# Kernel optimization log

Measured on AMD Instinct MI355X. Metric: run time of the kernel, lower is better.

## Reference

```python
import jax, jax.numpy as jnp
import numpy as np

H = 512      # config.hidden_dim
N = 64       # batch
W = 512      # sentence length
K = 8        # decode steps = pointer_answers.size(1)
NEG_BIG = 1e10


def setup_inputs() -> dict:
    key = jax.random.key(0)
    ks = jax.random.split(key, 10)
    stdv = 1.0 / np.sqrt(H)
    u = lambda k_, shape, s: jax.random.uniform(k_, shape, jnp.float32, -s, s)
    return {
        "context": jax.random.normal(ks[0], (N, W, 2 * H), jnp.float32),
        "sentence_lens": jax.random.randint(ks[1], (N,), 1, W + 1),
        "pointer_answers": jax.random.randint(ks[2], (N, K), 0, W + 1),
        "V_w": u(ks[3], (H, 2 * H), 1.0 / np.sqrt(2 * H)),
        "W_w": u(ks[4], (H, H), stdv),
        "v": u(ks[5], (H,), stdv),
        "w_ih": u(ks[6], (3 * H, 2 * H), stdv),
        "w_hh": u(ks[7], (3 * H, H), stdv),
        "b_ih": u(ks[8], (3 * H,), stdv),
        "b_hh": u(ks[9], (3 * H,), stdv),
    }


def reference(context, sentence_lens, pointer_answers, V_w, W_w, v, w_ih, w_hh, b_ih, b_hh):
    n, w_len, two_h = context.shape
    h_dim = two_h // 2
    k = pointer_answers.shape[1]

    # encoder output permuted to (W, N, 2H)
    ctx = jnp.swapaxes(context, 0, 1)
    # faithful reproduction of: context_new[i] = (1 - (i >= lens+1)*1e10) * context[i]
    pos = jnp.arange(w_len)[:, None]                                  # (W, 1)
    factor = 1.0 - (pos >= sentence_lens[None, :] + 1).astype(context.dtype) * NEG_BIG  # (W, N)
    ctx_masked = ctx * factor[:, :, None]                             # (W, N, 2H)
    # appended zeros row -> (W+1, N, 2H)
    context_new = jnp.concatenate([ctx_masked, jnp.zeros((1, n, two_h), context.dtype)], axis=0)

    ctx_t = jnp.einsum('snd,hd->snh', context_new, V_w)               # (W+1, N, H) = V(context_new)

    h0 = jnp.zeros((n, h_dim), context.dtype)

    def step(h, _):
        f = jnp.tanh(ctx_t + (h @ W_w.T)[None])                       # (W+1, N, H)
        scores = jnp.einsum('snh,h->sn', f, v)                        # (W+1, N)
        beta = jax.nn.softmax(scores, axis=0)                         # softmax over positions
        aligned = jnp.einsum('sn,snd->nd', beta, context_new)         # (N, 2H)
        # torch GRUCell math
        gi = aligned @ w_ih.T + b_ih                                  # (N, 3H)
        gh = h @ w_hh.T + b_hh                                        # (N, 3H)
        ir, iz, inew = jnp.split(gi, 3, axis=1)
        hr, hz, hnew = jnp.split(gh, 3, axis=1)
        r = jax.nn.sigmoid(ir + hr)
        z = jax.nn.sigmoid(iz + hz)
        ncand = jnp.tanh(inew + r * hnew)
        h_new = (1.0 - z) * ncand + z * h
        return h_new, beta.T                                          # (N, W+1)

    _, betas = jax.lax.scan(step, h0, None, length=k)                 # (k, N, W+1)
    # torch: cat over steps then permute -> (N, k, W+1) -> (N*k, W+1)
    out = jnp.transpose(betas, (1, 0, 2)).reshape(n * k, w_len + 1)
    return out
```

## Files before the change

kernel.cpp:

```cpp
#include <hip/hip_runtime.h>

#define N_    64
#define W_    512
#define H_    512
#define S_    513
#define TWOH_ 1024
#define KS_   8
#define FIXCAP_ 131072

typedef short s16x8 __attribute__((ext_vector_type(8)));
typedef float f32x4 __attribute__((ext_vector_type(4)));
typedef _Float16 h16x8 __attribute__((ext_vector_type(8)));

__device__ __forceinline__ float tanh_fast(float x) {
  float xc = fminf(fmaxf(x, -15.0f), 15.0f);
  float e = __expf(2.0f * xc);
  return (e - 1.0f) / (e + 1.0f);
}
__device__ __forceinline__ float sigmoid_f(float x) {
  return 1.0f / (1.0f + __expf(-x));
}
__device__ __forceinline__ float wred_sum(float v) {
#pragma unroll
  for (int m = 32; m > 0; m >>= 1) v += __shfl_xor(v, m, 64);
  return v;
}
__device__ __forceinline__ float bf2f(unsigned short u) {
  return __uint_as_float(((unsigned)u) << 16);
}

__device__ __forceinline__ void gld_lds16(const void* g, void* s) {
  __builtin_amdgcn_global_load_lds((__attribute__((address_space(1))) void*)g,
                                   (__attribute__((address_space(3))) void*)s,
                                   16, 0, 0);
}

__global__ __launch_bounds__(256) void k_cvt(const float4* __restrict__ x,
                                             unsigned short* __restrict__ hi,
                                             unsigned short* __restrict__ lo,
                                             int n4) {
  for (int i = blockIdx.x * 256 + threadIdx.x; i < n4; i += gridDim.x * 256) {
    float4 v = x[i];
    float vs[4] = {v.x, v.y, v.z, v.w};
    unsigned short hb[4], lb[4];
#pragma unroll
    for (int j = 0; j < 4; ++j) {
      unsigned u = __float_as_uint(vs[j]);
      unsigned short h = (unsigned short)((u + 0x7FFFu + ((u >> 16) & 1u)) >> 16);
      float hf = __uint_as_float((unsigned)h << 16);
      float lf = vs[j] - hf;
      unsigned u2 = __float_as_uint(lf);
      unsigned short l = (unsigned short)((u2 + 0x7FFFu + ((u2 >> 16) & 1u)) >> 16);
      hb[j] = h; lb[j] = l;
    }
    ushort4 h4; h4.x = hb[0]; h4.y = hb[1]; h4.z = hb[2]; h4.w = hb[3];
    ushort4 l4; l4.x = lb[0]; l4.y = lb[1]; l4.z = lb[2]; l4.w = lb[3];
    ((ushort4*)hi)[i] = h4;
    ((ushort4*)lo)[i] = l4;
  }
}

__global__ __launch_bounds__(256, 2) void mfma_gemm(
    const unsigned short* __restrict__ Ahi, const unsigned short* __restrict__ Alo,
    const unsigned short* __restrict__ Bhi, const unsigned short* __restrict__ Blo,
    _Float16* __restrict__ C) {
  __shared__ unsigned short sAh[4096], sAl[4096], sBh[4096], sBl[4096];
  int bid = blockIdx.x;
  int swz = (bid & 7) * 128 + (bid >> 3);
  int mt = swz >> 2, nt = swz & 3;
  int m0 = mt * 128, n0 = nt * 128;
  int tid = threadIdx.x;
  int wave = tid >> 6, lane = tid & 63;
  int wr = wave >> 1, wc = wave & 1;
  int fr = lane & 15, fq = lane >> 4;
  int rA = tid >> 2;
  int cA = (tid & 3) * 8;

  f32x4 acc[4][4] = {};

  const size_t a_row0 = (size_t)(m0 + rA) << 10;
  const size_t a_row1 = (size_t)(m0 + rA + 64) << 10;
  const size_t b_row0 = (size_t)(n0 + rA) << 10;
  const size_t b_row1 = (size_t)(n0 + rA + 64) << 10;
  const int wofs = wave << 9;

  for (int k0 = 0; k0 < 1024; k0 += 32) {
    int off = k0 + cA;
    gld_lds16(Ahi + a_row0 + off, sAh + wofs);
    gld_lds16(Ahi + a_row1 + off, sAh + 2048 + wofs);
    gld_lds16(Alo + a_row0 + off, sAl + wofs);
    gld_lds16(Alo + a_row1 + off, sAl + 2048 + wofs);
    gld_lds16(Bhi + b_row0 + off, sBh + wofs);
    gld_lds16(Bhi + b_row1 + off, sBh + 2048 + wofs);
    gld_lds16(Blo + b_row0 + off, sBl + wofs);
    gld_lds16(Blo + b_row1 + off, sBl + 2048 + wofs);
    __syncthreads();
    s16x8 ah[4], av[4], bh[4], bv[4];
#pragma unroll
    for (int m = 0; m < 4; ++m) {
      int ar = (wr * 64 + m * 16 + fr) * 32 + fq * 8;
      ah[m] = *(const s16x8*)(sAh + ar);
      av[m] = *(const s16x8*)(sAl + ar);
    }
#pragma unroll
    for (int n = 0; n < 4; ++n) {
      int br = (wc * 64 + n * 16 + fr) * 32 + fq * 8;
      bh[n] = *(const s16x8*)(sBh + br);
      bv[n] = *(const s16x8*)(sBl + br);
    }
#pragma unroll
    for (int m = 0; m < 4; ++m)
#pragma unroll
      for (int n = 0; n < 4; ++n) {
        acc[m][n] = __builtin_amdgcn_mfma_f32_16x16x32_bf16(ah[m], bh[n], acc[m][n], 0, 0, 0);
        acc[m][n] = __builtin_amdgcn_mfma_f32_16x16x32_bf16(ah[m], bv[n], acc[m][n], 0, 0, 0);
        acc[m][n] = __builtin_amdgcn_mfma_f32_16x16x32_bf16(av[m], bh[n], acc[m][n], 0, 0, 0);
      }
    __syncthreads();
  }
#pragma unroll
  for (int m = 0; m < 4; ++m) {
    int gr0 = m0 + wr * 64 + m * 16 + fq * 4;
#pragma unroll
    for (int n = 0; n < 4; ++n) {
      int gc = n0 + wc * 64 + n * 16 + fr;
      _Float16* cp = C + (size_t)gr0 * 512 + gc;
#pragma unroll
      for (int r = 0; r < 4; ++r) cp[(size_t)r * 512] = (_Float16)acc[m][n][r];
    }
  }
}

__global__ __launch_bounds__(1024) void k_mscore(
    const int* __restrict__ slens, const float* __restrict__ vvec,
    const _Float16* __restrict__ Vc16, float* __restrict__ scores,
    int* __restrict__ fixcnt, int* __restrict__ fixlist) {
  int nb = blockIdx.x & 63, cb = blockIdx.x >> 6;
  int t = threadIdx.x;
  int len = slens[nb];
  int w = t >> 6, lane = t & 63;
  int hb = lane << 3;
  float4 v0 = *(const float4*)(vvec + hb);
  float4 v1 = *(const float4*)(vvec + hb + 4);
  float vv[8] = {v0.x, v0.y, v0.z, v0.w, v1.x, v1.y, v1.z, v1.w};
  int s0 = max(cb * 128, len + 1);
  int s_end = min((cb + 1) * 128, W_);
  for (int s = s0 + w; s < s_end; s += 16) {
    h16x8 x8 = *(const h16x8*)(Vc16 + ((size_t)nb * W_ + s) * H_ + hb);
    float acc = 0.0f;
#pragma unroll
    for (int i = 0; i < 8; ++i) {
      float vcv = (float)x8[i];
      if (fabsf(vcv) < 6e-5f) {
        int idx = atomicAdd(fixcnt, 1);
        if (idx < FIXCAP_) fixlist[idx] = (nb << 20) | (s << 10) | (hb + i);
      } else {
        acc += (vcv > 0.0f) ? -vv[i] : vv[i];
      }
    }
    acc = wred_sum(acc);
    if (lane == 0) scores[nb * S_ + s] = acc;
  }
}

__global__ __launch_bounds__(256) void k_fix(
    const float* __restrict__ ctx, const float* __restrict__ Vw,
    const float* __restrict__ vvec, const int* __restrict__ fixcnt,
    const int* __restrict__ fixlist, float* __restrict__ scores) {
  int wid = (blockIdx.x * 256 + threadIdx.x) >> 6;
  int lane = threadIdx.x & 63;
  int cnt = min(*fixcnt, FIXCAP_);
  for (int e = wid; e < cnt; e += 1024) {
    int pk = fixlist[e];
    int n = pk >> 20, s = (pk >> 10) & 1023, h = pk & 1023;
    const float* cr = ctx + ((size_t)n * W_ + s) * TWOH_ + lane * 16;
    const float* wr = Vw + (size_t)h * TWOH_ + lane * 16;
    double acc = 0.0;
#pragma unroll
    for (int i = 0; i < 16; ++i) acc += (double)cr[i] * (double)wr[i];
#pragma unroll
    for (int m = 32; m > 0; m >>= 1) acc += __shfl_xor(acc, m, 64);
    if (lane == 0) {
      float vh = vvec[h];
      float contrib = (acc > 0.0) ? -vh : ((acc < 0.0) ? vh : 0.0f);
      if (contrib != 0.0f) atomicAdd(&scores[n * S_ + s], contrib);
    }
  }
}

__global__ __launch_bounds__(1024) void k_prep2(
    const float* __restrict__ ctx, const int* __restrict__ slens,
    const float* __restrict__ scores, float* __restrict__ Cmask) {
  __shared__ float4 red4[16 * 64];
  int nb = blockIdx.x & 63, cb = blockIdx.x >> 6;
  int t = threadIdx.x;
  int len = slens[nb];
  int dl = t & 63, sl = t >> 6;
  int d4 = cb * 256 + dl * 4;
  const float4* cp = (const float4*)(ctx + (size_t)nb * W_ * TWOH_) + (d4 >> 2);
  float4 acc = make_float4(0.f, 0.f, 0.f, 0.f);
#pragma unroll 4
  for (int s = len + 1 + sl; s < W_; s += 16) {
    float ew = __expf(scores[nb * S_ + s]);
    float4 c4 = cp[(size_t)s * (TWOH_ / 4)];
    acc.x += ew * c4.x; acc.y += ew * c4.y;
    acc.z += ew * c4.z; acc.w += ew * c4.w;
  }
  red4[sl * 64 + dl] = acc;
  __syncthreads();
  if (sl == 0) {
    float4 s4 = red4[dl];
#pragma unroll
    for (int i = 1; i < 16; ++i) {
      float4 o = red4[i * 64 + dl];
      s4.x += o.x; s4.y += o.y; s4.z += o.z; s4.w += o.w;
    }
    s4.x *= -1.0e10f; s4.y *= -1.0e10f; s4.z *= -1.0e10f; s4.w *= -1.0e10f;
    *(float4*)(Cmask + nb * TWOH_ + d4) = s4;
  }
}

__global__ __launch_bounds__(1024) void k_hw(const float* __restrict__ hc,
                                             const float* __restrict__ Ww,
                                             float* __restrict__ hWb) {
  __shared__ float ww[8][512];
  int b = blockIdx.x;
  int t = threadIdx.x;
  int h0 = b * 8;
  for (int i = t; i < 8 * 512; i += 1024)
    ww[i >> 9][i & 511] = Ww[(size_t)(h0 + (i >> 9)) * H_ + (i & 511)];
  __syncthreads();
  int lane = t & 63;
  int hl = (t >> 6) & 7;
  int nh = t >> 9;
  const float* wr = &ww[hl][lane << 3];
  float4 w0 = *(const float4*)wr;
  float4 w1 = *(const float4*)(wr + 4);
  for (int n = nh * 32; n < nh * 32 + 32; n += 2) {
    const float* hr0 = hc + (size_t)n * H_ + (lane << 3);
    const float* hr1 = hr0 + H_;
    float4 a0 = *(const float4*)hr0;
    float4 a1 = *(const float4*)(hr0 + 4);
    float4 b0 = *(const float4*)hr1;
    float4 b1 = *(const float4*)(hr1 + 4);
    float acc0 = a0.x * w0.x + a0.y * w0.y + a0.z * w0.z + a0.w * w0.w +
                 a1.x * w1.x + a1.y * w1.y + a1.z * w1.z + a1.w * w1.w;
    float acc1 = b0.x * w0.x + b0.y * w0.y + b0.z * w0.z + b0.w * w0.w +
                 b1.x * w1.x + b1.y * w1.y + b1.z * w1.z + b1.w * w1.w;
    acc0 = wred_sum(acc0);
    acc1 = wred_sum(acc1);
    if (lane == 0) {
      hWb[(size_t)n * H_ + h0 + hl] = acc0;
      hWb[(size_t)(n + 1) * H_ + h0 + hl] = acc1;
    }
  }
}

__global__ __launch_bounds__(1024) void k_scores(
    const int* __restrict__ slens, const float* __restrict__ hWb,
    const _Float16* __restrict__ Vc16, const float* __restrict__ vvec,
    float* __restrict__ scores) {
  int nb = blockIdx.x & 63, cb = blockIdx.x >> 6;
  int t = threadIdx.x;
  int len = slens[nb];
  int smax = min(len, W_ - 1);
  int w = t >> 6, lane = t & 63;
  int hb = lane << 3;
  float4 h0 = *(const float4*)(hWb + nb * H_ + hb);
  float4 h1 = *(const float4*)(hWb + nb * H_ + hb + 4);
  float4 v0 = *(const float4*)(vvec + hb);
  float4 v1 = *(const float4*)(vvec + hb + 4);
  float hw[8] = {h0.x, h0.y, h0.z, h0.w, h1.x, h1.y, h1.z, h1.w};
  float vv[8] = {v0.x, v0.y, v0.z, v0.w, v1.x, v1.y, v1.z, v1.w};
  int s_end = min((cb + 1) * 128 - 1, smax);
  const _Float16* vcb = Vc16 + (size_t)nb * W_ * H_ + hb;
  int s = cb * 128 + w;
  for (; s + 48 <= s_end; s += 64) {
    h16x8 x0 = *(const h16x8*)(vcb + (size_t)s * H_);
    h16x8 x1 = *(const h16x8*)(vcb + (size_t)(s + 16) * H_);
    h16x8 x2 = *(const h16x8*)(vcb + (size_t)(s + 32) * H_);
    h16x8 x3 = *(const h16x8*)(vcb + (size_t)(s + 48) * H_);
    float a0 = 0.f, a1 = 0.f, a2 = 0.f, a3 = 0.f;
#pragma unroll
    for (int i = 0; i < 8; ++i) {
      a0 += tanh_fast((float)x0[i] + hw[i]) * vv[i];
      a1 += tanh_fast((float)x1[i] + hw[i]) * vv[i];
      a2 += tanh_fast((float)x2[i] + hw[i]) * vv[i];
      a3 += tanh_fast((float)x3[i] + hw[i]) * vv[i];
    }
    a0 = wred_sum(a0); a1 = wred_sum(a1);
    a2 = wred_sum(a2); a3 = wred_sum(a3);
    if (lane == 0) {
      scores[nb * S_ + s] = a0;
      scores[nb * S_ + s + 16] = a1;
      scores[nb * S_ + s + 32] = a2;
      scores[nb * S_ + s + 48] = a3;
    }
  }
  for (; s <= s_end; s += 16) {
    h16x8 x8 = *(const h16x8*)(vcb + (size_t)s * H_);
    float acc = 0.0f;
#pragma unroll
    for (int i = 0; i < 8; ++i) acc += tanh_fast((float)x8[i] + hw[i]) * vv[i];
    acc = wred_sum(acc);
    if (lane == 0) scores[nb * S_ + s] = acc;
  }
  if (cb == 3 && w == 15) {
    float acc = 0.0f;
#pragma unroll
    for (int i = 0; i < 8; ++i) acc += tanh_fast(hw[i]) * vv[i];
    acc = wred_sum(acc);
    if (lane == 0) scores[nb * S_ + W_] = acc;
  }
}

__global__ __launch_bounds__(1024) void k_soft_aligned(
    const unsigned short* __restrict__ ctxb, const int* __restrict__ slens,
    const float* __restrict__ scores, const float* __restrict__ Cmask,
    float* __restrict__ alignedb, float* __restrict__ out, int k) {
  __shared__ float beta[520];
  __shared__ float wsum[16];
  __shared__ float redl[32 * 32 * 8];
  int nb = blockIdx.x & 63, cb = blockIdx.x >> 6;
  int t = threadIdx.x;
  int len = slens[nb];
  int smax = min(len, W_ - 1);

  float e = (t < S_) ? __expf(scores[nb * S_ + t]) : 0.0f;
  float ws_ = wred_sum(e);
  if ((t & 63) == 0) wsum[t >> 6] = ws_;
  __syncthreads();
  float D = 0.0f;
#pragma unroll
  for (int i = 0; i < 16; ++i) D += wsum[i];
  if (t < S_) {
    float bt = e / D;
    beta[t] = bt;
    if (cb == 0) out[(size_t)(nb * KS_ + k) * S_ + t] = bt;
  }
  __syncthreads();

  int dl = t & 31, sl = t >> 5;
  int d8 = cb * 256 + dl * 8;
  const unsigned short* cp = ctxb + (size_t)nb * W_ * TWOH_ + d8;
  float a[8] = {};
  int s = sl;
  for (; s + 96 <= smax; s += 128) {
    float b0 = beta[s], b1 = beta[s + 32], b2 = beta[s + 64], b3 = beta[s + 96];
    s16x8 c0 = *(const s16x8*)(cp + (size_t)s * TWOH_);
    s16x8 c1 = *(const s16x8*)(cp + (size_t)(s + 32) * TWOH_);
    s16x8 c2 = *(const s16x8*)(cp + (size_t)(s + 64) * TWOH_);
    s16x8 c3 = *(const s16x8*)(cp + (size_t)(s + 96) * TWOH_);
#pragma unroll
    for (int i = 0; i < 8; ++i)
      a[i] += b0 * bf2f((unsigned short)c0[i]) + b1 * bf2f((unsigned short)c1[i]) +
              b2 * bf2f((unsigned short)c2[i]) + b3 * bf2f((unsigned short)c3[i]);
  }
  for (; s <= smax; s += 32) {
    float bt = beta[s];
    s16x8 c = *(const s16x8*)(cp + (size_t)s * TWOH_);
#pragma unroll
    for (int i = 0; i < 8; ++i) a[i] += bt * bf2f((unsigned short)c[i]);
  }
  float4* rp = (float4*)(redl + (sl * 32 + dl) * 8);
  rp[0] = make_float4(a[0], a[1], a[2], a[3]);
  rp[1] = make_float4(a[4], a[5], a[6], a[7]);
  __syncthreads();
  if (t < 32) {
    float s8[8] = {};
#pragma unroll 8
    for (int q = 0; q < 32; ++q) {
      const float* p = redl + (q * 32 + t) * 8;
#pragma unroll
      for (int i = 0; i < 8; ++i) s8[i] += p[i];
    }
    float coef = 1.0f / D;
    int d8o = cb * 256 + t * 8;
    const float* cmp = Cmask + nb * TWOH_ + d8o;
    float* ap = alignedb + nb * TWOH_ + d8o;
#pragma unroll
    for (int i = 0; i < 8; ++i) ap[i] = s8[i] + coef * cmp[i];
  }
}

__global__ __launch_bounds__(1024) void k_gru(
    const float* __restrict__ alignedb, const float* __restrict__ hc,
    const float* __restrict__ wih, const float* __restrict__ whh,
    const float* __restrict__ bih, const float* __restrict__ bhh,
    float* __restrict__ hnx) {
  __shared__ float ls_wih[6 * TWOH_];
  __shared__ float ls_whh[6 * H_];
  __shared__ float part[8 * 128 * 6];
  int b = blockIdx.x;
  int t = threadIdx.x;
  const int j0 = 2 * b;
  for (int i = t; i < 6 * TWOH_; i += 1024) {
    int row = i >> 10, d = i & 1023;
    int jl = row / 3, g = row - jl * 3;
    ls_wih[i] = wih[(size_t)(g * H_ + j0 + jl) * TWOH_ + d];
  }
  for (int i = t; i < 6 * H_; i += 1024) {
    int row = i >> 9, d = i & 511;
    int jl = row / 3, g = row - jl * 3;
    ls_whh[i] = whh[(size_t)(g * H_ + j0 + jl) * H_ + d];
  }
  __syncthreads();
  int nj = t & 127, sl = t >> 7;
  int n = nj & 63, jl = nj >> 6;
  const float* ar = alignedb + n * TWOH_ + sl * 128;
  const float* hr = hc + n * H_ + sl * 64;
  const float* w0 = ls_wih + (jl * 3 + 0) * TWOH_ + sl * 128;
  const float* w1 = ls_wih + (jl * 3 + 1) * TWOH_ + sl * 128;
  const float* w2 = ls_wih + (jl * 3 + 2) * TWOH_ + sl * 128;
  const float* u0 = ls_whh + (jl * 3 + 0) * H_ + sl * 64;
  const float* u1 = ls_whh + (jl * 3 + 1) * H_ + sl * 64;
  const float* u2 = ls_whh + (jl * 3 + 2) * H_ + sl * 64;
  float g0 = 0.f, g1 = 0.f, g2 = 0.f;
#pragma unroll 8
  for (int i = 0; i < 128; i += 4) {
    float4 a4 = *(const float4*)(ar + i);
    g0 += a4.x * w0[i] + a4.y * w0[i + 1] + a4.z * w0[i + 2] + a4.w * w0[i + 3];
    g1 += a4.x * w1[i] + a4.y * w1[i + 1] + a4.z * w1[i + 2] + a4.w * w1[i + 3];
    g2 += a4.x * w2[i] + a4.y * w2[i + 1] + a4.z * w2[i + 2] + a4.w * w2[i + 3];
  }
  float q0 = 0.f, q1 = 0.f, q2 = 0.f;
#pragma unroll 8
  for (int i = 0; i < 64; i += 4) {
    float4 h4 = *(const float4*)(hr + i);
    q0 += h4.x * u0[i] + h4.y * u0[i + 1] + h4.z * u0[i + 2] + h4.w * u0[i + 3];
    q1 += h4.x * u1[i] + h4.y * u1[i + 1] + h4.z * u1[i + 2] + h4.w * u1[i + 3];
    q2 += h4.x * u2[i] + h4.y * u2[i + 1] + h4.z * u2[i + 2] + h4.w * u2[i + 3];
  }
  float* pp = part + (sl * 128 + nj) * 6;
  pp[0] = g0; pp[1] = g1; pp[2] = g2; pp[3] = q0; pp[4] = q1; pp[5] = q2;
  __syncthreads();
  if (t < 128) {
    int n2 = t & 63, jl2 = t >> 6;
    int j = j0 + jl2;
    float G0 = 0.f, G1 = 0.f, G2 = 0.f, Q0 = 0.f, Q1 = 0.f, Q2 = 0.f;
#pragma unroll
    for (int s = 0; s < 8; ++s) {
      float* p = part + (s * 128 + t) * 6;
      G0 += p[0]; G1 += p[1]; G2 += p[2];
      Q0 += p[3]; Q1 += p[4]; Q2 += p[5];
    }
    float r = sigmoid_f(G0 + bih[j] + Q0 + bhh[j]);
    float z = sigmoid_f(G1 + bih[H_ + j] + Q1 + bhh[H_ + j]);
    float nc = tanh_fast(G2 + bih[2 * H_ + j] + r * (Q2 + bhh[2 * H_ + j]));
    hnx[n2 * H_ + j] = (1.0f - z) * nc + z * hc[n2 * H_ + j];
  }
}

extern "C" void kernel_launch(void* const* d_in, const int* in_sizes, int n_in,
                              void* d_out, int out_size, void* d_ws, size_t ws_size,
                              hipStream_t stream) {
  const float* ctx = (const float*)d_in[0];
  const int* slens = (const int*)d_in[1];
  const float* Vw = (const float*)d_in[3];
  const float* Ww = (const float*)d_in[4];
  const float* vvec = (const float*)d_in[5];
  const float* wih = (const float*)d_in[6];
  const float* whh = (const float*)d_in[7];
  const float* bih = (const float*)d_in[8];
  const float* bhh = (const float*)d_in[9];
  float* out = (float*)d_out;

  char* p = (char*)d_ws;
  _Float16* Vc16 = (_Float16*)p;      p += (size_t)N_ * W_ * H_ * 2;
  float* scores = (float*)p;          p += (size_t)N_ * S_ * 4;
  int* fixcnt = (int*)p;              p += 256;
  int* fixlist = (int*)p;             p += (size_t)FIXCAP_ * 4;
  float* Cm = (float*)p;              p += (size_t)N_ * TWOH_ * 4;
  float* hb = (float*)p;              p += (size_t)2 * N_ * H_ * 4;
  float* hWb = (float*)p;             p += (size_t)N_ * H_ * 4;
  float* al = (float*)p;              p += (size_t)N_ * TWOH_ * 4;
  unsigned short* Ahi = (unsigned short*)p;  p += (size_t)32768 * 1024 * 2;
  unsigned short* Alo = (unsigned short*)p;  p += (size_t)32768 * 1024 * 2;
  unsigned short* Bhi = (unsigned short*)p;  p += (size_t)512 * 1024 * 2;
  unsigned short* Blo = (unsigned short*)p;  p += (size_t)512 * 1024 * 2;
  size_t need = (size_t)(p - (char*)d_ws);
  if (ws_size < need) return;

  hipMemsetAsync(hb, 0, (size_t)N_ * H_ * sizeof(float), stream);
  hipMemsetAsync(fixcnt, 0, sizeof(int), stream);
  k_cvt<<<2048, 256, 0, stream>>>((const float4*)ctx, Ahi, Alo, 8388608);
  k_cvt<<<512, 256, 0, stream>>>((const float4*)Vw, Bhi, Blo, 131072);
  mfma_gemm<<<1024, 256, 0, stream>>>(Ahi, Alo, Bhi, Blo, Vc16);
  k_mscore<<<256, 1024, 0, stream>>>(slens, vvec, Vc16, scores, fixcnt, fixlist);
  k_fix<<<256, 256, 0, stream>>>(ctx, Vw, vvec, fixcnt, fixlist, scores);
  k_prep2<<<256, 1024, 0, stream>>>(ctx, slens, scores, Cm);

  for (int k = 0; k < KS_; ++k) {
    const float* hc = hb + (k & 1) * (N_ * H_);
    float* hn = hb + ((k + 1) & 1) * (N_ * H_);
    k_hw<<<64, 1024, 0, stream>>>(hc, Ww, hWb);
    k_scores<<<256, 1024, 0, stream>>>(slens, hWb, Vc16, vvec, scores);
    k_soft_aligned<<<256, 1024, 0, stream>>>(Ahi, slens, scores, Cm, al, out, k);
    k_gru<<<256, 1024, 0, stream>>>(al, hc, wih, whh, bih, bhh, hn);
  }
}
```

Measured before the change: 692.7 us.

## Fuse masked-score pass into GEMM epilogue, merge conversions, double grid sizes

```diff
diff --git a/kernel.cpp b/kernel.cpp
--- a/kernel.cpp
+++ b/kernel.cpp
@@ -35,12 +35,15 @@
                                    16, 0, 0);
 }
 
-__global__ __launch_bounds__(256) void k_cvt(const float4* __restrict__ x,
-                                             unsigned short* __restrict__ hi,
-                                             unsigned short* __restrict__ lo,
-                                             int n4) {
-  for (int i = blockIdx.x * 256 + threadIdx.x; i < n4; i += gridDim.x * 256) {
-    float4 v = x[i];
+__global__ __launch_bounds__(256) void k_cvt2(
+    const float4* __restrict__ xa, unsigned short* __restrict__ Ahi,
+    unsigned short* __restrict__ Alo, const float4* __restrict__ xb,
+    unsigned short* __restrict__ Bhi, unsigned short* __restrict__ Blo) {
+  const int NA = 8388608;
+  const int NT = NA + 131072;
+  for (int i = blockIdx.x * 256 + threadIdx.x; i < NT; i += gridDim.x * 256) {
+    bool isA = (i < NA);
+    float4 v = isA ? xa[i] : xb[i - NA];
     float vs[4] = {v.x, v.y, v.z, v.w};
     unsigned short hb[4], lb[4];
 #pragma unroll
@@ -55,15 +58,22 @@
     }
     ushort4 h4; h4.x = hb[0]; h4.y = hb[1]; h4.z = hb[2]; h4.w = hb[3];
     ushort4 l4; l4.x = lb[0]; l4.y = lb[1]; l4.z = lb[2]; l4.w = lb[3];
-    ((ushort4*)hi)[i] = h4;
-    ((ushort4*)lo)[i] = l4;
+    if (isA) {
+      ((ushort4*)Ahi)[i] = h4;
+      ((ushort4*)Alo)[i] = l4;
+    } else {
+      ((ushort4*)Bhi)[i - NA] = h4;
+      ((ushort4*)Blo)[i - NA] = l4;
+    }
   }
 }
 
 __global__ __launch_bounds__(256, 2) void mfma_gemm(
     const unsigned short* __restrict__ Ahi, const unsigned short* __restrict__ Alo,
     const unsigned short* __restrict__ Bhi, const unsigned short* __restrict__ Blo,
-    _Float16* __restrict__ C) {
+    _Float16* __restrict__ C, const int* __restrict__ slens,
+    const float* __restrict__ vvec, float* __restrict__ scores,
+    int* __restrict__ fixcnt, int* __restrict__ fixlist) {
   __shared__ unsigned short sAh[4096], sAl[4096], sBh[4096], sBl[4096];
   int bid = blockIdx.x;
   int swz = (bid & 7) * 128 + (bid >> 3);
@@ -118,48 +128,50 @@
       }
     __syncthreads();
   }
+
+  const int n_batch = m0 >> 9;
+  const int len = slens[n_batch];
+  const int s_tile0 = m0 & 511;
+  const bool any_masked = (s_tile0 + 127 >= len + 1);
+  float vv4[4];
+#pragma unroll
+  for (int nf = 0; nf < 4; ++nf) vv4[nf] = vvec[n0 + wc * 64 + nf * 16 + fr];
+
 #pragma unroll
   for (int m = 0; m < 4; ++m) {
     int gr0 = m0 + wr * 64 + m * 16 + fq * 4;
 #pragma unroll
-    for (int n = 0; n < 4; ++n) {
-      int gc = n0 + wc * 64 + n * 16 + fr;
+    for (int nf = 0; nf < 4; ++nf) {
+      int gc = n0 + wc * 64 + nf * 16 + fr;
       _Float16* cp = C + (size_t)gr0 * 512 + gc;
 #pragma unroll
-      for (int r = 0; r < 4; ++r) cp[(size_t)r * 512] = (_Float16)acc[m][n][r];
-    }
-  }
-}
-
-__global__ __launch_bounds__(1024) void k_mscore(
-    const int* __restrict__ slens, const float* __restrict__ vvec,
-    const _Float16* __restrict__ Vc16, float* __restrict__ scores,
-    int* __restrict__ fixcnt, int* __restrict__ fixlist) {
-  int nb = blockIdx.x & 63, cb = blockIdx.x >> 6;
-  int t = threadIdx.x;
-  int len = slens[nb];
-  int w = t >> 6, lane = t & 63;
-  int hb = lane << 3;
-  float4 v0 = *(const float4*)(vvec + hb);
-  float4 v1 = *(const float4*)(vvec + hb + 4);
-  float vv[8] = {v0.x, v0.y, v0.z, v0.w, v1.x, v1.y, v1.z, v1.w};
-  int s0 = max(cb * 128, len + 1);
-  int s_end = min((cb + 1) * 128, W_);
-  for (int s = s0 + w; s < s_end; s += 16) {
-    h16x8 x8 = *(const h16x8*)(Vc16 + ((size_t)nb * W_ + s) * H_ + hb);
-    float acc = 0.0f;
-#pragma unroll
-    for (int i = 0; i < 8; ++i) {
-      float vcv = (float)x8[i];
-      if (fabsf(vcv) < 6e-5f) {
-        int idx = atomicAdd(fixcnt, 1);
-        if (idx < FIXCAP_) fixlist[idx] = (nb << 20) | (s << 10) | (hb + i);
-      } else {
-        acc += (vcv > 0.0f) ? -vv[i] : vv[i];
+      for (int r = 0; r < 4; ++r) cp[(size_t)r * 512] = (_Float16)acc[m][nf][r];
+    }
+    if (any_masked) {
+#pragma unroll
+      for (int r = 0; r < 4; ++r) {
+        int s_row = (gr0 + r) & 511;
+        if (s_row >= len + 1) {
+          float part = 0.0f;
+#pragma unroll
+          for (int nf = 0; nf < 4; ++nf) {
+            float a = acc[m][nf][r];
+            if (fabsf(a) <= 1e-5f) {
+              int gc = n0 + wc * 64 + nf * 16 + fr;
+              int idx = atomicAdd(fixcnt, 1);
+              if (idx < FIXCAP_) fixlist[idx] = (n_batch << 20) | (s_row << 10) | gc;
+            } else {
+              part += (a > 0.0f) ? -vv4[nf] : vv4[nf];
+            }
+          }
+          part += __shfl_xor(part, 1, 64);
+          part += __shfl_xor(part, 2, 64);
+          part += __shfl_xor(part, 4, 64);
+          part += __shfl_xor(part, 8, 64);
+          if (fr == 0) atomicAdd(&scores[n_batch * S_ + s_row], part);
+        }
       }
     }
-    acc = wred_sum(acc);
-    if (lane == 0) scores[nb * S_ + s] = acc;
   }
 }
 
@@ -223,20 +235,20 @@
 __global__ __launch_bounds__(1024) void k_hw(const float* __restrict__ hc,
                                              const float* __restrict__ Ww,
                                              float* __restrict__ hWb) {
-  __shared__ float ww[8][512];
+  __shared__ float ww[4][512];
   int b = blockIdx.x;
   int t = threadIdx.x;
-  int h0 = b * 8;
-  for (int i = t; i < 8 * 512; i += 1024)
+  int h0 = b * 4;
+  for (int i = t; i < 4 * 512; i += 1024)
     ww[i >> 9][i & 511] = Ww[(size_t)(h0 + (i >> 9)) * H_ + (i & 511)];
   __syncthreads();
   int lane = t & 63;
-  int hl = (t >> 6) & 7;
-  int nh = t >> 9;
+  int hl = (t >> 6) & 3;
+  int nh = t >> 8;
   const float* wr = &ww[hl][lane << 3];
   float4 w0 = *(const float4*)wr;
   float4 w1 = *(const float4*)(wr + 4);
-  for (int n = nh * 32; n < nh * 32 + 32; n += 2) {
+  for (int n = nh * 16; n < nh * 16 + 16; n += 2) {
     const float* hr0 = hc + (size_t)n * H_ + (lane << 3);
     const float* hr1 = hr0 + H_;
     float4 a0 = *(const float4*)hr0;
@@ -272,29 +284,22 @@
   float4 v1 = *(const float4*)(vvec + hb + 4);
   float hw[8] = {h0.x, h0.y, h0.z, h0.w, h1.x, h1.y, h1.z, h1.w};
   float vv[8] = {v0.x, v0.y, v0.z, v0.w, v1.x, v1.y, v1.z, v1.w};
-  int s_end = min((cb + 1) * 128 - 1, smax);
+  int s_end = min((cb + 1) * 64 - 1, smax);
   const _Float16* vcb = Vc16 + (size_t)nb * W_ * H_ + hb;
-  int s = cb * 128 + w;
-  for (; s + 48 <= s_end; s += 64) {
+  int s = cb * 64 + w;
+  for (; s + 16 <= s_end; s += 32) {
     h16x8 x0 = *(const h16x8*)(vcb + (size_t)s * H_);
     h16x8 x1 = *(const h16x8*)(vcb + (size_t)(s + 16) * H_);
-    h16x8 x2 = *(const h16x8*)(vcb + (size_t)(s + 32) * H_);
-    h16x8 x3 = *(const h16x8*)(vcb + (size_t)(s + 48) * H_);
-    float a0 = 0.f, a1 = 0.f, a2 = 0.f, a3 = 0.f;
+    float a0 = 0.f, a1 = 0.f;
 #pragma unroll
     for (int i = 0; i < 8; ++i) {
       a0 += tanh_fast((float)x0[i] + hw[i]) * vv[i];
       a1 += tanh_fast((float)x1[i] + hw[i]) * vv[i];
-      a2 += tanh_fast((float)x2[i] + hw[i]) * vv[i];
-      a3 += tanh_fast((float)x3[i] + hw[i]) * vv[i];
     }
     a0 = wred_sum(a0); a1 = wred_sum(a1);
-    a2 = wred_sum(a2); a3 = wred_sum(a3);
     if (lane == 0) {
       scores[nb * S_ + s] = a0;
       scores[nb * S_ + s + 16] = a1;
-      scores[nb * S_ + s + 32] = a2;
-      scores[nb * S_ + s + 48] = a3;
     }
   }
   for (; s <= s_end; s += 16) {
@@ -305,7 +310,7 @@
     acc = wred_sum(acc);
     if (lane == 0) scores[nb * S_ + s] = acc;
   }
-  if (cb == 3 && w == 15) {
+  if (cb == 7 && w == 15) {
     float acc = 0.0f;
 #pragma unroll
     for (int i = 0; i < 8; ++i) acc += tanh_fast(hw[i]) * vv[i];
@@ -320,7 +325,7 @@
     float* __restrict__ alignedb, float* __restrict__ out, int k) {
   __shared__ float beta[520];
   __shared__ float wsum[16];
-  __shared__ float redl[32 * 32 * 8];
+  __shared__ float redl[64 * 16 * 8];
   int nb = blockIdx.x & 63, cb = blockIdx.x >> 6;
   int t = threadIdx.x;
   int len = slens[nb];
@@ -340,46 +345,36 @@
   }
   __syncthreads();
 
-  int dl = t & 31, sl = t >> 5;
-  int d8 = cb * 256 + dl * 8;
+  int dl = t & 15, sl = t >> 4;
+  int d8 = cb * 128 + dl * 8;
   const unsigned short* cp = ctxb + (size_t)nb * W_ * TWOH_ + d8;
   float a[8] = {};
   int s = sl;
-  for (; s + 96 <= smax; s += 128) {
-    float b0 = beta[s], b1 = beta[s + 32], b2 = beta[s + 64], b3 = beta[s + 96];
+  for (; s + 64 <= smax; s += 128) {
+    float b0 = beta[s], b1 = beta[s + 64];
     s16x8 c0 = *(const s16x8*)(cp + (size_t)s * TWOH_);
-    s16x8 c1 = *(const s16x8*)(cp + (size_t)(s + 32) * TWOH_);
-    s16x8 c2 = *(const s16x8*)(cp + (size_t)(s + 64) * TWOH_);
-    s16x8 c3 = *(const s16x8*)(cp + (size_t)(s + 96) * TWOH_);
+    s16x8 c1 = *(const s16x8*)(cp + (size_t)(s + 64) * TWOH_);
 #pragma unroll
     for (int i = 0; i < 8; ++i)
-      a[i] += b0 * bf2f((unsigned short)c0[i]) + b1 * bf2f((unsigned short)c1[i]) +
-              b2 * bf2f((unsigned short)c2[i]) + b3 * bf2f((unsigned short)c3[i]);
-  }
-  for (; s <= smax; s += 32) {
+      a[i] += b0 * bf2f((unsigned short)c0[i]) + b1 * bf2f((unsigned short)c1[i]);
+  }
+  for (; s <= smax; s += 64) {
     float bt = beta[s];
     s16x8 c = *(const s16x8*)(cp + (size_t)s * TWOH_);
 #pragma unroll
     for (int i = 0; i < 8; ++i) a[i] += bt * bf2f((unsigned short)c[i]);
   }
-  float4* rp = (float4*)(redl + (sl * 32 + dl) * 8);
+  float4* rp = (float4*)(redl + sl * 128 + dl * 8);
   rp[0] = make_float4(a[0], a[1], a[2], a[3]);
   rp[1] = make_float4(a[4], a[5], a[6], a[7]);
   __syncthreads();
-  if (t < 32) {
-    float s8[8] = {};
-#pragma unroll 8
-    for (int q = 0; q < 32; ++q) {
-      const float* p = redl + (q * 32 + t) * 8;
-#pragma unroll
-      for (int i = 0; i < 8; ++i) s8[i] += p[i];
-    }
+  if (t < 128) {
+    float ssum = 0.0f;
+#pragma unroll 16
+    for (int q = 0; q < 64; ++q) ssum += redl[q * 128 + t];
     float coef = 1.0f / D;
-    int d8o = cb * 256 + t * 8;
-    const float* cmp = Cmask + nb * TWOH_ + d8o;
-    float* ap = alignedb + nb * TWOH_ + d8o;
-#pragma unroll
-    for (int i = 0; i < 8; ++i) ap[i] = s8[i] + coef * cmp[i];
+    int dd = nb * TWOH_ + cb * 128 + t;
+    alignedb[dd] = ssum + coef * Cmask[dd];
   }
 }
 
@@ -483,19 +478,20 @@
 
   hipMemsetAsync(hb, 0, (size_t)N_ * H_ * sizeof(float), stream);
   hipMemsetAsync(fixcnt, 0, sizeof(int), stream);
-  k_cvt<<<2048, 256, 0, stream>>>((const float4*)ctx, Ahi, Alo, 8388608);
-  k_cvt<<<512, 256, 0, stream>>>((const float4*)Vw, Bhi, Blo, 131072);
-  mfma_gemm<<<1024, 256, 0, stream>>>(Ahi, Alo, Bhi, Blo, Vc16);
-  k_mscore<<<256, 1024, 0, stream>>>(slens, vvec, Vc16, scores, fixcnt, fixlist);
+  hipMemsetAsync(scores, 0, (size_t)N_ * S_ * sizeof(float), stream);
+  k_cvt2<<<2048, 256, 0, stream>>>((const float4*)ctx, Ahi, Alo,
+                                   (const float4*)Vw, Bhi, Blo);
+  mfma_gemm<<<1024, 256, 0, stream>>>(Ahi, Alo, Bhi, Blo, Vc16, slens, vvec,
+                                      scores, fixcnt, fixlist);
   k_fix<<<256, 256, 0, stream>>>(ctx, Vw, vvec, fixcnt, fixlist, scores);
   k_prep2<<<256, 1024, 0, stream>>>(ctx, slens, scores, Cm);
 
   for (int k = 0; k < KS_; ++k) {
     const float* hc = hb + (k & 1) * (N_ * H_);
     float* hn = hb + ((k + 1) & 1) * (N_ * H_);
-    k_hw<<<64, 1024, 0, stream>>>(hc, Ww, hWb);
-    k_scores<<<256, 1024, 0, stream>>>(slens, hWb, Vc16, vvec, scores);
-    k_soft_aligned<<<256, 1024, 0, stream>>>(Ahi, slens, scores, Cm, al, out, k);
+    k_hw<<<128, 1024, 0, stream>>>(hc, Ww, hWb);
+    k_scores<<<512, 1024, 0, stream>>>(slens, hWb, Vc16, vvec, scores);
+    k_soft_aligned<<<512, 1024, 0, stream>>>(Ahi, slens, scores, Cm, al, out, k);
     k_gru<<<256, 1024, 0, stream>>>(al, hc, wih, whh, bih, bhh, hn);
   }
 }
```

Measured after the change: 653.9 us. 1.06x faster.
